# Performance work log

Hardware: AMD Instinct MI355X
Metric: run time of the kernel (lower is better)

The kernel has to match this reference:

```python
import jax, jax.numpy as jnp
import numpy as np

N = 40000      # nodes
E = 640000     # edges
F_IN = 128     # features_channels
H = 512        # GraphConv hidden
G = 64         # graphs in batch


def _glorot(key, shape):
    fan_in, fan_out = shape
    lim = float(np.sqrt(6.0 / (fan_in + fan_out)))
    return jax.random.uniform(key, shape, jnp.float32, -lim, lim)


def setup_inputs() -> dict:
    key = jax.random.key(0)
    ks = jax.random.split(key, 16)
    x = jax.random.normal(ks[0], (N, F_IN), jnp.float32)
    edge_index = jax.random.randint(ks[1], (2, E), 0, N, jnp.int64)
    edge_attr = jax.random.uniform(ks[2], (E,), jnp.float32)
    batch = jnp.sort(jax.random.randint(ks[3], (N,), 0, G, jnp.int64))
    return {
        "x": x, "edge_index": edge_index, "edge_attr": edge_attr, "batch": batch,
        # GraphConv1: lin_rel (with bias) on aggregated msgs, lin_root (no bias) on x
        "W_rel1": _glorot(ks[4], (F_IN, H)), "b_rel1": jnp.zeros((H,), jnp.float32),
        "W_root1": _glorot(ks[5], (F_IN, H)),
        "W_rel2": _glorot(ks[6], (H, H)), "b_rel2": jnp.zeros((H,), jnp.float32),
        "W_root2": _glorot(ks[7], (H, H)),
        # dense head
        "W1": _glorot(ks[8], (H, 64)), "b1": jnp.zeros((64,), jnp.float32),
        "W2": _glorot(ks[9], (64, 16)), "b2": jnp.zeros((16,), jnp.float32),
        "W3": _glorot(ks[10], (16, 1)), "b3": jnp.zeros((1,), jnp.float32),
    }


def _graph_conv(x, src, dst, ew, W_rel, b_rel, W_root):
    # PyG GraphConv (aggr='add'): out = lin_rel(sum_{j->i} w_ij * x_j) + lin_root(x_i)
    msg = x[src] * ew[:, None]                              # [E, C]
    agg = jax.ops.segment_sum(msg, dst, num_segments=N)     # [N, C]
    return agg @ W_rel + b_rel + x @ W_root


def reference(x, edge_index, edge_attr, batch,
              W_rel1, b_rel1, W_root1, W_rel2, b_rel2, W_root2,
              W1, b1, W2, b2, W3, b3):
    src, dst = edge_index[0], edge_index[1]
    h = jax.nn.relu(_graph_conv(x, src, dst, edge_attr, W_rel1, b_rel1, W_root1))
    h = jax.nn.relu(_graph_conv(h, src, dst, edge_attr, W_rel2, b_rel2, W_root2))
    # global_mean_pool over graph ids
    sums = jax.ops.segment_sum(h, batch, num_segments=G)            # [G, H]
    cnts = jax.ops.segment_sum(jnp.ones((N,), h.dtype), batch, num_segments=G)
    pooled = sums / jnp.maximum(cnts, 1.0)[:, None]
    # dropout is identity in eval mode
    o = jax.nn.relu(pooled @ W1 + b1)
    o = jax.nn.relu(o @ W2 + b2)
    return o @ W3 + b3                                               # [G, 1]
```

## Files before the change

kernel.cpp:

```cpp
#include <hip/hip_runtime.h>
#include <hip/hip_bf16.h>
#include <hip/hip_fp8.h>

#define NNODES 40000
#define MPAD   40192
#define NEDGES 640000
#define FIN    128
#define HID    512
#define NGRAPH 64

typedef __attribute__((ext_vector_type(8))) short bf16x8;
typedef __attribute__((ext_vector_type(4))) float f32x4;
typedef __attribute__((ext_vector_type(2))) float f32x2;

__device__ __forceinline__ unsigned short f2bf(float f) {
    unsigned int u = __builtin_bit_cast(unsigned int, f);
    u += 0x7FFFu + ((u >> 16) & 1u);
    return (unsigned short)(u >> 16);
}
__device__ __forceinline__ float bf2f(unsigned short s) {
    return __builtin_bit_cast(float, (unsigned int)s << 16);
}

__device__ __forceinline__ unsigned char f2fp8(float v) {
#if __has_builtin(__builtin_amdgcn_cvt_pk_fp8_f32)
    int p = __builtin_amdgcn_cvt_pk_fp8_f32(v, v, 0, false);
    return (unsigned char)(p & 0xFF);
#else
    __hip_fp8_e4m3 q(v);
    return (unsigned char)q.__x;
#endif
}
template <bool HI>
__device__ __forceinline__ f32x2 fp8pair2f(int word) {
#if __has_builtin(__builtin_amdgcn_cvt_pk_f32_fp8)
    return __builtin_amdgcn_cvt_pk_f32_fp8(word, HI);
#else
    f32x2 r;
    __hip_fp8_e4m3 a, b;
    a.__x = (unsigned char)((word >> (HI ? 16 : 0)) & 0xFF);
    b.__x = (unsigned char)((word >> (HI ? 24 : 8)) & 0xFF);
    r.x = (float)a; r.y = (float)b;
    return r;
#endif
}

__device__ __forceinline__ void gload_lds16(const void* g, void* l) {
    __builtin_amdgcn_global_load_lds(
        (const __attribute__((address_space(1))) void*)g,
        (__attribute__((address_space(3))) void*)l, 16, 0, 0);
}

#define DS_READ_B128(dst, addr, OFF) \
    asm volatile("ds_read_b128 %0, %1 offset:" OFF : "=v"(dst) : "v"(addr))


__global__ void k_cvt_x(const float* __restrict__ x, unsigned short* __restrict__ xb) {
    size_t e = ((size_t)blockIdx.x * 256 + threadIdx.x) * 8;
    if (e >= (size_t)MPAD * FIN) return;
    bf16x8 o;
    if (e < (size_t)NNODES * FIN) {
        float4 v0 = *(const float4*)(x + e);
        float4 v1 = *(const float4*)(x + e + 4);
        o[0] = f2bf(v0.x); o[1] = f2bf(v0.y); o[2] = f2bf(v0.z); o[3] = f2bf(v0.w);
        o[4] = f2bf(v1.x); o[5] = f2bf(v1.y); o[6] = f2bf(v1.z); o[7] = f2bf(v1.w);
    } else {
        o = (bf16x8)0;
    }
    *(bf16x8*)(xb + e) = o;
}

__global__ void k_cvt_wt(const float* __restrict__ W, unsigned short* __restrict__ Wt, int K) {
    int t = blockIdx.x * 256 + threadIdx.x;
    if (t >= 512 * K) return;
    int n = t / K, k = t - n * K;
    Wt[t] = f2bf(W[(size_t)k * 512 + n]);
}


__global__ void k_deg(const int* __restrict__ dst, int* __restrict__ deg) {
    int e = blockIdx.x * 256 + threadIdx.x;
    if (e < NEDGES) atomicAdd(&deg[dst[e]], 1);
}

__global__ void k_scan(const int* __restrict__ deg, int* __restrict__ off, int* __restrict__ cursor) {
    __shared__ int sh[1024];
    constexpr int CH = (NNODES + 1023) / 1024;
    int t = threadIdx.x;
    int base = t * CH;
    int vals[CH];
    int local = 0;
#pragma unroll
    for (int i = 0; i < CH; ++i) {
        int idx = base + i;
        int v = (idx < NNODES) ? deg[idx] : 0;
        vals[i] = v;
        local += v;
    }
    sh[t] = local;
    __syncthreads();
    for (int o = 1; o < 1024; o <<= 1) {
        int add = (t >= o) ? sh[t - o] : 0;
        __syncthreads();
        sh[t] += add;
        __syncthreads();
    }
    int run = sh[t] - local;
#pragma unroll
    for (int i = 0; i < CH; ++i) {
        int idx = base + i;
        if (idx < NNODES) {
            off[idx] = run;
            cursor[idx] = run;
            run += vals[i];
        }
    }
    if (t == 1023) off[NNODES] = sh[1023];
}

__global__ void k_fill(const int* __restrict__ src, const int* __restrict__ dst,
                       const float* __restrict__ ew, int* __restrict__ cursor,
                       int* __restrict__ csrc, float* __restrict__ cw) {
    int e = blockIdx.x * 256 + threadIdx.x;
    if (e < NEDGES) {
        int p = atomicAdd(&cursor[dst[e]], 1);
        csrc[p] = src[e];
        cw[p] = ew[e];
    }
}


__global__ void k_agg128(const unsigned short* __restrict__ xb, const int* __restrict__ off,
                         const int* __restrict__ csrc, const float* __restrict__ cw,
                         unsigned short* __restrict__ out) {
    int node = blockIdx.x * 4 + (threadIdx.x >> 6);
    if (node >= NNODES) return;
    int lane = threadIdx.x & 63;
    float a0 = 0.f, a1 = 0.f;
    int s = off[node], e = off[node + 1];
    for (int k = s; k < e; ++k) {
        int j = csrc[k];
        float w = cw[k];
        unsigned int v = *(const unsigned int*)(xb + (size_t)j * FIN + lane * 2);
        a0 += w * bf2f((unsigned short)(v & 0xFFFF));
        a1 += w * bf2f((unsigned short)(v >> 16));
    }
    unsigned int o = (unsigned int)f2bf(a0) | ((unsigned int)f2bf(a1) << 16);
    *(unsigned int*)(out + (size_t)node * FIN + lane * 2) = o;
}

__global__ void k_agg512(const unsigned char* __restrict__ h8, const int* __restrict__ off,
                         const int* __restrict__ csrc, const float* __restrict__ cw,
                         unsigned short* __restrict__ out) {
    int node = blockIdx.x * 4 + (threadIdx.x >> 6);
    if (node >= NNODES) return;
    int lane = threadIdx.x & 63;
    float acc[8] = {};
    int s = off[node], e = off[node + 1];
    for (int k = s; k < e; ++k) {
        int j = csrc[k];
        float w = cw[k];
        int2 v = *(const int2*)(h8 + (size_t)j * HID + lane * 8);
        f32x2 f01 = fp8pair2f<false>(v.x);
        f32x2 f23 = fp8pair2f<true>(v.x);
        f32x2 f45 = fp8pair2f<false>(v.y);
        f32x2 f67 = fp8pair2f<true>(v.y);
        acc[0] += w * f01.x; acc[1] += w * f01.y;
        acc[2] += w * f23.x; acc[3] += w * f23.y;
        acc[4] += w * f45.x; acc[5] += w * f45.y;
        acc[6] += w * f67.x; acc[7] += w * f67.y;
    }
    bf16x8 o;
#pragma unroll
    for (int q = 0; q < 8; ++q) o[q] = (short)f2bf(acc[q]);
    *(bf16x8*)(out + (size_t)node * HID + lane * 8) = o;
}


template <int K, bool POOL>
__global__ __launch_bounds__(512, 2)
void k_mfma_dual(const unsigned short* __restrict__ A0, const unsigned short* __restrict__ B0t,
                 const unsigned short* __restrict__ A1, const unsigned short* __restrict__ B1t,
                 const float* __restrict__ bias,
                 unsigned short* __restrict__ C, unsigned char* __restrict__ C8,
                 const int* __restrict__ batch, float* __restrict__ psum) {
    constexpr int KT = K / 32;
    constexpr int S = 2 * KT;
    __shared__ unsigned short As[4][256 * 32];
    __shared__ unsigned short Bs[4][256 * 32];
    int tid = threadIdx.x;
    int l = tid & 63, w = tid >> 6;
    int wr = w >> 2, wc = w & 3;
    int bid = blockIdx.x;
    int row0 = (bid >> 1) * 256;
    int col0 = (bid & 1) * 256;

    int lr = l & 15, hi = l >> 4;
    int pofs = (hi ^ ((lr >> 1) & 3)) * 8;

    const unsigned short* Amat[2] = {A0, A1};
    const unsigned short* Bmat[2] = {B0t, B1t};

    int c0 = tid, c1 = tid + 512;
    int r0 = c0 >> 2, g0 = (c0 & 3) ^ ((r0 >> 1) & 3);
    int r1 = c1 >> 2, g1 = (c1 & 3) ^ ((r1 >> 1) & 3);

    auto stage_half = [&](int s, int half) {
        int mat = s / KT;
        int k0 = (s - mat * KT) * 32;
        const unsigned short* A = Amat[mat];
        const unsigned short* Bt = Bmat[mat];
        int c = half ? c1 : c0;
        int r = half ? r1 : r0;
        int g = half ? g1 : g0;
        gload_lds16(A + (size_t)(row0 + r) * K + k0 + g * 8, &As[s & 3][c * 8]);
        gload_lds16(Bt + (size_t)(col0 + r) * K + k0 + g * 8, &Bs[s & 3][c * 8]);
    };

    unsigned a_lane = (unsigned)(unsigned long long)&As[0][0]
                    + (unsigned)(((wr * 128 + lr) * 32 + pofs) * 2);
    unsigned b_lane = (unsigned)(unsigned long long)&Bs[0][0]
                    + (unsigned)(((wc * 64 + lr) * 32 + pofs) * 2);

    f32x4 acc[8][4];
#pragma unroll
    for (int m = 0; m < 8; ++m)
#pragma unroll
        for (int n = 0; n < 4; ++n) acc[m][n] = (f32x4)0.f;

    stage_half(0, 0); stage_half(0, 1);
    stage_half(1, 0); stage_half(1, 1);
    asm volatile("s_waitcnt vmcnt(4)" ::: "memory");
    __builtin_amdgcn_s_barrier();
    __builtin_amdgcn_sched_barrier(0);

    for (int s = 0; s < S; ++s) {
        if (s + 2 < S) {
            stage_half(s + 2, 0);
            stage_half(s + 2, 1);
        }
        unsigned ab = a_lane + (unsigned)((s & 3) * (256 * 32 * 2));
        unsigned bb = b_lane + (unsigned)((s & 3) * (256 * 32 * 2));
        bf16x8 af[8], bfr[4];
        DS_READ_B128(af[0], ab, "0");
        DS_READ_B128(af[1], ab, "1024");
        DS_READ_B128(af[2], ab, "2048");
        DS_READ_B128(af[3], ab, "3072");
        DS_READ_B128(af[4], ab, "4096");
        DS_READ_B128(af[5], ab, "5120");
        DS_READ_B128(af[6], ab, "6144");
        DS_READ_B128(af[7], ab, "7168");
        DS_READ_B128(bfr[0], bb, "0");
        DS_READ_B128(bfr[1], bb, "1024");
        DS_READ_B128(bfr[2], bb, "2048");
        DS_READ_B128(bfr[3], bb, "3072");
        asm volatile("s_waitcnt lgkmcnt(0)" ::: "memory");
        __builtin_amdgcn_sched_barrier(0);
        __builtin_amdgcn_s_setprio(1);
#pragma unroll
        for (int m = 0; m < 4; ++m)
#pragma unroll
            for (int n = 0; n < 4; ++n)
                acc[m][n] = __builtin_amdgcn_mfma_f32_16x16x32_bf16(af[m], bfr[n], acc[m][n], 0, 0, 0);
        __builtin_amdgcn_s_setprio(0);
        __builtin_amdgcn_s_setprio(1);
#pragma unroll
        for (int m = 0; m < 4; ++m)
#pragma unroll
            for (int n = 0; n < 4; ++n)
                acc[4 + m][n] = __builtin_amdgcn_mfma_f32_16x16x32_bf16(af[4 + m], bfr[n], acc[4 + m][n], 0, 0, 0);
        __builtin_amdgcn_s_setprio(0);
        if (s + 2 < S) {
            asm volatile("s_waitcnt vmcnt(4)" ::: "memory");
        } else {
            asm volatile("s_waitcnt vmcnt(0)" ::: "memory");
        }
        if (s + 1 < S) {
            __builtin_amdgcn_s_barrier();
            __builtin_amdgcn_sched_barrier(0);
        }
    }

    float bv[4];
#pragma unroll
    for (int n = 0; n < 4; ++n) bv[n] = bias[col0 + wc * 64 + n * 16 + lr];
    int rbase = row0 + wr * 128 + hi * 4;

    if constexpr (!POOL) {
#pragma unroll
        for (int m = 0; m < 8; ++m) {
#pragma unroll
            for (int i = 0; i < 4; ++i) {
                int rr = rbase + m * 16 + i;
                if (rr < NNODES) {
#pragma unroll
                    for (int n = 0; n < 4; ++n) {
                        int col = col0 + wc * 64 + n * 16 + lr;
                        float v = fmaxf(acc[m][n][i] + bv[n], 0.f);
                        C[(size_t)rr * HID + col] = f2bf(v);
                        C8[(size_t)rr * HID + col] = f2fp8(v);
                    }
                }
            }
        }
    } else {
#pragma unroll
        for (int m = 0; m < 8; ++m) {
            int b[4];
#pragma unroll
            for (int i = 0; i < 4; ++i) {
                int rr = rbase + m * 16 + i;
                b[i] = (rr < NNODES) ? batch[rr] : -1;
            }
#pragma unroll
            for (int n = 0; n < 4; ++n) {
                int col = col0 + wc * 64 + n * 16 + lr;
                int cb = -1;
                float run = 0.f;
#pragma unroll
                for (int i = 0; i < 4; ++i) {
                    if (b[i] >= 0) {
                        float v = fmaxf(acc[m][n][i] + bv[n], 0.f);
                        if (b[i] == cb) {
                            run += v;
                        } else {
                            if (cb >= 0) atomicAdd(&psum[(size_t)cb * HID + col], run);
                            cb = b[i];
                            run = v;
                        }
                    }
                }
                if (cb >= 0) atomicAdd(&psum[(size_t)cb * HID + col], run);
            }
        }
    }
}


__global__ void k_cnt(const int* __restrict__ batch, float* __restrict__ cnt) {
    __shared__ int h[NGRAPH];
    int t = threadIdx.x;
    if (t < NGRAPH) h[t] = 0;
    __syncthreads();
    int i = blockIdx.x * 256 + t;
    if (i < NNODES) atomicAdd(&h[batch[i]], 1);
    __syncthreads();
    if (t < NGRAPH && h[t] != 0) atomicAdd(&cnt[t], (float)h[t]);
}

__global__ void k_head(const float* __restrict__ psum, const float* __restrict__ cnt,
                       const float* __restrict__ W1, const float* __restrict__ b1,
                       const float* __restrict__ W2, const float* __restrict__ b2,
                       const float* __restrict__ W3, const float* __restrict__ b3,
                       float* __restrict__ out) {
    __shared__ float pooled[HID];
    __shared__ float o1[64];
    __shared__ float o2[16];
    int g = blockIdx.x, t = threadIdx.x;
    float c = fmaxf(cnt[g], 1.0f);
    for (int k = t; k < HID; k += 64) pooled[k] = psum[(size_t)g * HID + k] / c;
    __syncthreads();
    float a = b1[t];
    for (int k = 0; k < HID; ++k) a += pooled[k] * W1[k * 64 + t];
    o1[t] = fmaxf(a, 0.f);
    __syncthreads();
    if (t < 16) {
        float a2 = b2[t];
        for (int k = 0; k < 64; ++k) a2 += o1[k] * W2[k * 16 + t];
        o2[t] = fmaxf(a2, 0.f);
    }
    __syncthreads();
    if (t == 0) {
        float a3 = b3[0];
        for (int k = 0; k < 16; ++k) a3 += o2[k] * W3[k];
        out[g] = a3;
    }
}


extern "C" void kernel_launch(void* const* d_in, const int* in_sizes, int n_in,
                              void* d_out, int out_size, void* d_ws, size_t ws_size,
                              hipStream_t stream) {
    const float* x = (const float*)d_in[0];
    const int* ei = (const int*)d_in[1];
    const int* src = ei;
    const int* dst = ei + NEDGES;
    const float* ew = (const float*)d_in[2];
    const int* batch = (const int*)d_in[3];
    const float* Wr1 = (const float*)d_in[4];
    const float* br1 = (const float*)d_in[5];
    const float* Wo1 = (const float*)d_in[6];
    const float* Wr2 = (const float*)d_in[7];
    const float* br2 = (const float*)d_in[8];
    const float* Wo2 = (const float*)d_in[9];
    const float* W1 = (const float*)d_in[10];
    const float* b1 = (const float*)d_in[11];
    const float* W2 = (const float*)d_in[12];
    const float* b2 = (const float*)d_in[13];
    const float* W3 = (const float*)d_in[14];
    const float* b3 = (const float*)d_in[15];
    float* out = (float*)d_out;

    char* ws = (char*)d_ws;
    size_t o = 0;
    auto alloc = [&](size_t bytes) -> void* {
        void* p = ws + o;
        o = (o + bytes + 255) & ~(size_t)255;
        return p;
    };
    int* deg = (int*)alloc((size_t)NNODES * 4);
    int* off = (int*)alloc((size_t)(NNODES + 1) * 4);
    int* cur = (int*)alloc((size_t)NNODES * 4);
    int* csrc = (int*)alloc((size_t)NEDGES * 4);
    float* cw = (float*)alloc((size_t)NEDGES * 4);
    unsigned short* xb = (unsigned short*)alloc((size_t)MPAD * FIN * 2);
    unsigned short* agg1 = (unsigned short*)alloc((size_t)MPAD * FIN * 2);
    unsigned short* h1 = (unsigned short*)alloc((size_t)MPAD * HID * 2);
    unsigned char* h1f8 = (unsigned char*)alloc((size_t)MPAD * HID);
    unsigned short* agg2 = (unsigned short*)alloc((size_t)MPAD * HID * 2);
    unsigned short* Wr1t = (unsigned short*)alloc((size_t)512 * FIN * 2);
    unsigned short* Wo1t = (unsigned short*)alloc((size_t)512 * FIN * 2);
    unsigned short* Wr2t = (unsigned short*)alloc((size_t)512 * HID * 2);
    unsigned short* Wo2t = (unsigned short*)alloc((size_t)512 * HID * 2);
    float* psum = (float*)alloc((size_t)NGRAPH * HID * 4);
    float* cnt = (float*)alloc((size_t)NGRAPH * 4);

    hipMemsetAsync(deg, 0, (size_t)NNODES * 4, stream);
    hipMemsetAsync(psum, 0, (size_t)NGRAPH * HID * 4, stream);
    hipMemsetAsync(cnt, 0, (size_t)NGRAPH * 4, stream);

    k_cvt_x<<<((MPAD * FIN / 8) + 255) / 256, 256, 0, stream>>>(x, xb);
    k_cvt_wt<<<(512 * FIN + 255) / 256, 256, 0, stream>>>(Wr1, Wr1t, FIN);
    k_cvt_wt<<<(512 * FIN + 255) / 256, 256, 0, stream>>>(Wo1, Wo1t, FIN);
    k_cvt_wt<<<(512 * HID + 255) / 256, 256, 0, stream>>>(Wr2, Wr2t, HID);
    k_cvt_wt<<<(512 * HID + 255) / 256, 256, 0, stream>>>(Wo2, Wo2t, HID);

    k_deg<<<(NEDGES + 255) / 256, 256, 0, stream>>>(dst, deg);
    k_scan<<<1, 1024, 0, stream>>>(deg, off, cur);
    k_fill<<<(NEDGES + 255) / 256, 256, 0, stream>>>(src, dst, ew, cur, csrc, cw);

    k_agg128<<<(NNODES + 3) / 4, 256, 0, stream>>>(xb, off, csrc, cw, agg1);
    int nblk = (MPAD / 256) * 2;
    k_mfma_dual<FIN, false><<<nblk, 512, 0, stream>>>(agg1, Wr1t, xb, Wo1t, br1, h1, h1f8, nullptr, nullptr);

    k_agg512<<<(NNODES + 3) / 4, 256, 0, stream>>>(h1f8, off, csrc, cw, agg2);
    k_cnt<<<(NNODES + 255) / 256, 256, 0, stream>>>(batch, cnt);
    k_mfma_dual<HID, true><<<nblk, 512, 0, stream>>>(agg2, Wr2t, h1, Wo2t, br2, nullptr, nullptr, batch, psum);

    k_head<<<NGRAPH, 64, 0, stream>>>(psum, cnt, W1, b1, W2, b2, W3, b3, out);
}
```

Before: 454.5 us.

## Use 160-row GEMM tiles without padding and unroll edge gathers by four

The dual GEMM tile height drops from 256 to 160 rows, so 40000 nodes divide evenly and the padded rows go away (MPAD becomes 40000). That gives 500 blocks instead of 314, which should balance better across CUs. A-tile staging now uses 4-byte global-to-LDS loads to fit the new row mapping, which issues more load instructions per stage. Both aggregation kernels also unroll the edge loop by four so more independent gathers are in flight.

```diff
diff --git a/kernel.cpp b/kernel.cpp
--- a/kernel.cpp
+++ b/kernel.cpp
@@ -3,11 +3,12 @@
 #include <hip/hip_fp8.h>
 
 #define NNODES 40000
-#define MPAD   40192
+#define MPAD   40000
 #define NEDGES 640000
 #define FIN    128
 #define HID    512
 #define NGRAPH 64
+#define BM     160
 
 typedef __attribute__((ext_vector_type(8))) short bf16x8;
 typedef __attribute__((ext_vector_type(4))) float f32x4;
@@ -50,6 +51,11 @@
         (const __attribute__((address_space(1))) void*)g,
         (__attribute__((address_space(3))) void*)l, 16, 0, 0);
 }
+__device__ __forceinline__ void gload_lds4(const void* g, void* l) {
+    __builtin_amdgcn_global_load_lds(
+        (const __attribute__((address_space(1))) void*)g,
+        (__attribute__((address_space(3))) void*)l, 4, 0, 0);
+}
 
 #define DS_READ_B128(dst, addr, OFF) \
     asm volatile("ds_read_b128 %0, %1 offset:" OFF : "=v"(dst) : "v"(addr))
@@ -58,15 +64,11 @@
 __global__ void k_cvt_x(const float* __restrict__ x, unsigned short* __restrict__ xb) {
     size_t e = ((size_t)blockIdx.x * 256 + threadIdx.x) * 8;
     if (e >= (size_t)MPAD * FIN) return;
+    float4 v0 = *(const float4*)(x + e);
+    float4 v1 = *(const float4*)(x + e + 4);
     bf16x8 o;
-    if (e < (size_t)NNODES * FIN) {
-        float4 v0 = *(const float4*)(x + e);
-        float4 v1 = *(const float4*)(x + e + 4);
-        o[0] = f2bf(v0.x); o[1] = f2bf(v0.y); o[2] = f2bf(v0.z); o[3] = f2bf(v0.w);
-        o[4] = f2bf(v1.x); o[5] = f2bf(v1.y); o[6] = f2bf(v1.z); o[7] = f2bf(v1.w);
-    } else {
-        o = (bf16x8)0;
-    }
+    o[0] = f2bf(v0.x); o[1] = f2bf(v0.y); o[2] = f2bf(v0.z); o[3] = f2bf(v0.w);
+    o[4] = f2bf(v1.x); o[5] = f2bf(v1.y); o[6] = f2bf(v1.z); o[7] = f2bf(v1.w);
     *(bf16x8*)(xb + e) = o;
 }
 
@@ -138,7 +140,20 @@
     int lane = threadIdx.x & 63;
     float a0 = 0.f, a1 = 0.f;
     int s = off[node], e = off[node + 1];
-    for (int k = s; k < e; ++k) {
+    int k = s;
+    for (; k + 3 < e; k += 4) {
+        int j0 = csrc[k], j1 = csrc[k + 1], j2 = csrc[k + 2], j3 = csrc[k + 3];
+        float w0 = cw[k], w1 = cw[k + 1], w2 = cw[k + 2], w3 = cw[k + 3];
+        unsigned int v0 = *(const unsigned int*)(xb + (size_t)j0 * FIN + lane * 2);
+        unsigned int v1 = *(const unsigned int*)(xb + (size_t)j1 * FIN + lane * 2);
+        unsigned int v2 = *(const unsigned int*)(xb + (size_t)j2 * FIN + lane * 2);
+        unsigned int v3 = *(const unsigned int*)(xb + (size_t)j3 * FIN + lane * 2);
+        a0 += w0 * bf2f((unsigned short)(v0 & 0xFFFF)); a1 += w0 * bf2f((unsigned short)(v0 >> 16));
+        a0 += w1 * bf2f((unsigned short)(v1 & 0xFFFF)); a1 += w1 * bf2f((unsigned short)(v1 >> 16));
+        a0 += w2 * bf2f((unsigned short)(v2 & 0xFFFF)); a1 += w2 * bf2f((unsigned short)(v2 >> 16));
+        a0 += w3 * bf2f((unsigned short)(v3 & 0xFFFF)); a1 += w3 * bf2f((unsigned short)(v3 >> 16));
+    }
+    for (; k < e; ++k) {
         int j = csrc[k];
         float w = cw[k];
         unsigned int v = *(const unsigned int*)(xb + (size_t)j * FIN + lane * 2);
@@ -157,10 +172,7 @@
     int lane = threadIdx.x & 63;
     float acc[8] = {};
     int s = off[node], e = off[node + 1];
-    for (int k = s; k < e; ++k) {
-        int j = csrc[k];
-        float w = cw[k];
-        int2 v = *(const int2*)(h8 + (size_t)j * HID + lane * 8);
+    auto accum = [&](int2 v, float w) {
         f32x2 f01 = fp8pair2f<false>(v.x);
         f32x2 f23 = fp8pair2f<true>(v.x);
         f32x2 f45 = fp8pair2f<false>(v.y);
@@ -169,6 +181,20 @@
         acc[2] += w * f23.x; acc[3] += w * f23.y;
         acc[4] += w * f45.x; acc[5] += w * f45.y;
         acc[6] += w * f67.x; acc[7] += w * f67.y;
+    };
+    int k = s;
+    for (; k + 3 < e; k += 4) {
+        int j0 = csrc[k], j1 = csrc[k + 1], j2 = csrc[k + 2], j3 = csrc[k + 3];
+        float w0 = cw[k], w1 = cw[k + 1], w2 = cw[k + 2], w3 = cw[k + 3];
+        int2 v0 = *(const int2*)(h8 + (size_t)j0 * HID + lane * 8);
+        int2 v1 = *(const int2*)(h8 + (size_t)j1 * HID + lane * 8);
+        int2 v2 = *(const int2*)(h8 + (size_t)j2 * HID + lane * 8);
+        int2 v3 = *(const int2*)(h8 + (size_t)j3 * HID + lane * 8);
+        accum(v0, w0); accum(v1, w1); accum(v2, w2); accum(v3, w3);
+    }
+    for (; k < e; ++k) {
+        int2 v = *(const int2*)(h8 + (size_t)csrc[k] * HID + lane * 8);
+        accum(v, cw[k]);
     }
     bf16x8 o;
 #pragma unroll
@@ -186,13 +212,13 @@
                  const int* __restrict__ batch, float* __restrict__ psum) {
     constexpr int KT = K / 32;
     constexpr int S = 2 * KT;
-    __shared__ unsigned short As[4][256 * 32];
+    __shared__ unsigned short As[4][BM * 32];
     __shared__ unsigned short Bs[4][256 * 32];
     int tid = threadIdx.x;
     int l = tid & 63, w = tid >> 6;
     int wr = w >> 2, wc = w & 3;
     int bid = blockIdx.x;
-    int row0 = (bid >> 1) * 256;
+    int row0 = (bid >> 1) * BM;
     int col0 = (bid & 1) * 256;
 
     int lr = l & 15, hi = l >> 4;
@@ -201,55 +227,54 @@
     const unsigned short* Amat[2] = {A0, A1};
     const unsigned short* Bmat[2] = {B0t, B1t};
 
-    int c0 = tid, c1 = tid + 512;
-    int r0 = c0 >> 2, g0 = (c0 & 3) ^ ((r0 >> 1) & 3);
-    int r1 = c1 >> 2, g1 = (c1 & 3) ^ ((r1 >> 1) & 3);
-
-    auto stage_half = [&](int s, int half) {
+    int bc0 = tid, bc1 = tid + 512;
+    int br0 = bc0 >> 2, bg0 = (bc0 & 3) ^ ((br0 >> 1) & 3);
+    int br1 = bc1 >> 2, bg1 = (bc1 & 3) ^ ((br1 >> 1) & 3);
+
+    auto stage = [&](int s) {
         int mat = s / KT;
         int k0 = (s - mat * KT) * 32;
         const unsigned short* A = Amat[mat];
         const unsigned short* Bt = Bmat[mat];
-        int c = half ? c1 : c0;
-        int r = half ? r1 : r0;
-        int g = half ? g1 : g0;
-        gload_lds16(A + (size_t)(row0 + r) * K + k0 + g * 8, &As[s & 3][c * 8]);
-        gload_lds16(Bt + (size_t)(col0 + r) * K + k0 + g * 8, &Bs[s & 3][c * 8]);
+        gload_lds16(Bt + (size_t)(col0 + br0) * K + k0 + bg0 * 8, &Bs[s & 3][bc0 * 8]);
+        gload_lds16(Bt + (size_t)(col0 + br1) * K + k0 + bg1 * 8, &Bs[s & 3][bc1 * 8]);
+#pragma unroll
+        for (int q = 0; q < 5; ++q) {
+            int c = tid + q * 512;
+            int r = c >> 4;
+            int g = ((c >> 2) & 3) ^ ((r >> 1) & 3);
+            int u = c & 3;
+            gload_lds4(A + (size_t)(row0 + r) * K + k0 + g * 8 + u * 2, &As[s & 3][c * 2]);
+        }
     };
 
     unsigned a_lane = (unsigned)(unsigned long long)&As[0][0]
-                    + (unsigned)(((wr * 128 + lr) * 32 + pofs) * 2);
+                    + (unsigned)(((wr * 80 + lr) * 32 + pofs) * 2);
     unsigned b_lane = (unsigned)(unsigned long long)&Bs[0][0]
                     + (unsigned)(((wc * 64 + lr) * 32 + pofs) * 2);
 
-    f32x4 acc[8][4];
-#pragma unroll
-    for (int m = 0; m < 8; ++m)
+    f32x4 acc[5][4];
+#pragma unroll
+    for (int m = 0; m < 5; ++m)
 #pragma unroll
         for (int n = 0; n < 4; ++n) acc[m][n] = (f32x4)0.f;
 
-    stage_half(0, 0); stage_half(0, 1);
-    stage_half(1, 0); stage_half(1, 1);
-    asm volatile("s_waitcnt vmcnt(4)" ::: "memory");
+    stage(0);
+    stage(1);
+    asm volatile("s_waitcnt vmcnt(7)" ::: "memory");
     __builtin_amdgcn_s_barrier();
     __builtin_amdgcn_sched_barrier(0);
 
     for (int s = 0; s < S; ++s) {
-        if (s + 2 < S) {
-            stage_half(s + 2, 0);
-            stage_half(s + 2, 1);
-        }
-        unsigned ab = a_lane + (unsigned)((s & 3) * (256 * 32 * 2));
+        if (s + 2 < S) stage(s + 2);
+        unsigned ab = a_lane + (unsigned)((s & 3) * (BM * 32 * 2));
         unsigned bb = b_lane + (unsigned)((s & 3) * (256 * 32 * 2));
-        bf16x8 af[8], bfr[4];
+        bf16x8 af[5], bfr[4];
         DS_READ_B128(af[0], ab, "0");
         DS_READ_B128(af[1], ab, "1024");
         DS_READ_B128(af[2], ab, "2048");
         DS_READ_B128(af[3], ab, "3072");
         DS_READ_B128(af[4], ab, "4096");
-        DS_READ_B128(af[5], ab, "5120");
-        DS_READ_B128(af[6], ab, "6144");
-        DS_READ_B128(af[7], ab, "7168");
         DS_READ_B128(bfr[0], bb, "0");
         DS_READ_B128(bfr[1], bb, "1024");
         DS_READ_B128(bfr[2], bb, "2048");
@@ -258,20 +283,20 @@
         __builtin_amdgcn_sched_barrier(0);
         __builtin_amdgcn_s_setprio(1);
 #pragma unroll
-        for (int m = 0; m < 4; ++m)
+        for (int m = 0; m < 3; ++m)
 #pragma unroll
             for (int n = 0; n < 4; ++n)
                 acc[m][n] = __builtin_amdgcn_mfma_f32_16x16x32_bf16(af[m], bfr[n], acc[m][n], 0, 0, 0);
         __builtin_amdgcn_s_setprio(0);
         __builtin_amdgcn_s_setprio(1);
 #pragma unroll
-        for (int m = 0; m < 4; ++m)
+        for (int m = 3; m < 5; ++m)
 #pragma unroll
             for (int n = 0; n < 4; ++n)
-                acc[4 + m][n] = __builtin_amdgcn_mfma_f32_16x16x32_bf16(af[4 + m], bfr[n], acc[4 + m][n], 0, 0, 0);
+                acc[m][n] = __builtin_amdgcn_mfma_f32_16x16x32_bf16(af[m], bfr[n], acc[m][n], 0, 0, 0);
         __builtin_amdgcn_s_setprio(0);
         if (s + 2 < S) {
-            asm volatile("s_waitcnt vmcnt(4)" ::: "memory");
+            asm volatile("s_waitcnt vmcnt(7)" ::: "memory");
         } else {
             asm volatile("s_waitcnt vmcnt(0)" ::: "memory");
         }
@@ -284,11 +309,11 @@
     float bv[4];
 #pragma unroll
     for (int n = 0; n < 4; ++n) bv[n] = bias[col0 + wc * 64 + n * 16 + lr];
-    int rbase = row0 + wr * 128 + hi * 4;
+    int rbase = row0 + wr * 80 + hi * 4;
 
     if constexpr (!POOL) {
 #pragma unroll
-        for (int m = 0; m < 8; ++m) {
+        for (int m = 0; m < 5; ++m) {
 #pragma unroll
             for (int i = 0; i < 4; ++i) {
                 int rr = rbase + m * 16 + i;
@@ -305,7 +330,7 @@
         }
     } else {
 #pragma unroll
-        for (int m = 0; m < 8; ++m) {
+        for (int m = 0; m < 5; ++m) {
             int b[4];
 #pragma unroll
             for (int i = 0; i < 4; ++i) {
@@ -440,7 +465,7 @@
     k_fill<<<(NEDGES + 255) / 256, 256, 0, stream>>>(src, dst, ew, cur, csrc, cw);
 
     k_agg128<<<(NNODES + 3) / 4, 256, 0, stream>>>(xb, off, csrc, cw, agg1);
-    int nblk = (MPAD / 256) * 2;
+    int nblk = (MPAD / BM) * 2;
     k_mfma_dual<FIN, false><<<nblk, 512, 0, stream>>>(agg1, Wr1t, xb, Wo1t, br1, h1, h1f8, nullptr, nullptr);
 
     k_agg512<<<(NNODES + 3) / 4, 256, 0, stream>>>(h1f8, off, csrc, cw, agg2);
```

After: 379.8 us. -16.4%, faster.
